# Kernel tuning notes

Hardware: AMD Instinct MI355X
Metric: run time of the kernel (lower is better)

The kernel has to match this reference:

```python
import jax, jax.numpy as jnp
import numpy as np

N, M, F, B = 100000, 12, 64, 41  # atoms, max neighbors, atom feat dim, bond feat dim
EPS = 1e-5


def setup_inputs() -> dict:
    key = jax.random.key(0)
    ks = jax.random.split(key, 8)
    neighbor_indices = jax.random.randint(ks[0], (N, M), 0, N, dtype=jnp.int32)
    atom_features = jax.random.normal(ks[1], (N, F), dtype=jnp.float32)
    bond_features = jax.random.normal(ks[2], (N, M, B), dtype=jnp.float32)
    W = jax.random.normal(ks[3], (2 * F + B, 2 * F), dtype=jnp.float32) * 0.05
    b = jnp.zeros((2 * F,), dtype=jnp.float32)
    bn1_scale = 1.0 + 0.02 * jax.random.normal(ks[4], (2 * F,), dtype=jnp.float32)
    bn1_offset = 0.02 * jax.random.normal(ks[5], (2 * F,), dtype=jnp.float32)
    bn2_scale = 1.0 + 0.02 * jax.random.normal(ks[6], (F,), dtype=jnp.float32)
    bn2_offset = 0.02 * jax.random.normal(ks[7], (F,), dtype=jnp.float32)
    return {"neighbor_indices": neighbor_indices, "atom_features": atom_features,
            "bond_features": bond_features, "W": W, "b": b,
            "bn1_scale": bn1_scale, "bn1_offset": bn1_offset,
            "bn2_scale": bn2_scale, "bn2_offset": bn2_offset}


def batchnorm(x, scale, offset):
    # haiku BatchNorm, training mode: batch stats over all axes but channel (last)
    mean = jnp.mean(x, axis=0, keepdims=True)
    var = jnp.mean(jnp.square(x), axis=0, keepdims=True) - jnp.square(mean)
    inv = scale * jax.lax.rsqrt(var + EPS)
    return (x - mean) * inv + offset


def reference(neighbor_indices, atom_features, bond_features, W, b,
              bn1_scale, bn1_offset, bn2_scale, bn2_offset):
    n = atom_features.shape[0]
    nbr_feats = atom_features[neighbor_indices]  # (N, M, F) gather
    self_feats = jnp.broadcast_to(atom_features[:, None, :], (n, M, F))
    total = jnp.concatenate([self_feats, nbr_feats, bond_features], axis=2)  # (N, M, 2F+B)
    gated = total @ W + b  # (N, M, 2F)
    gated = batchnorm(gated.reshape(-1, 2 * F), bn1_scale, bn1_offset).reshape(n, M, 2 * F)
    nbr_filter, nbr_core = jnp.split(gated, 2, axis=2)
    summed = jnp.sum(jax.nn.sigmoid(nbr_filter) * jax.nn.softplus(nbr_core), axis=1)  # (N, F)
    summed = batchnorm(summed, bn2_scale, bn2_offset)
    return jax.nn.softplus(atom_features + summed)
```

## Files before the change

### kernel.cpp

```cpp
#include <hip/hip_runtime.h>
#include <hip/hip_bf16.h>
#include <math.h>


#define NATOMS  100000
#define MNBR    12
#define FDIM    64
#define BDIM    41
#define C2F     128
#define EPSBN   1e-5f
#define NBLK    2048
#define GROUPS  (NATOMS/4)
#define AR      136
#define PR      72

typedef __attribute__((ext_vector_type(8))) short  short8;
typedef __attribute__((ext_vector_type(4))) float  f32x4;

__device__ __forceinline__ float softplusf(float x) {
    return fmaxf(x, 0.f) + __logf(1.f + __expf(-fabsf(x)));
}
__device__ __forceinline__ float sigmoidf(float x) {
    return 1.f / (1.f + __expf(-x));
}
__device__ __forceinline__ unsigned short f2bf(float f) {
    unsigned int x = __builtin_bit_cast(unsigned int, f);
    unsigned int r = (x + 0x7fff + ((x >> 16) & 1)) >> 16;
    return (unsigned short)r;
}
__device__ __forceinline__ unsigned int pkbf(float a, float b) {
    unsigned short lo = __builtin_bit_cast(unsigned short, __float2bfloat16(a));
    unsigned short hi = __builtin_bit_cast(unsigned short, __float2bfloat16(b));
    return (unsigned)lo | ((unsigned)hi << 16);
}
__device__ __forceinline__ float bflo(unsigned int u) {
    return __builtin_bit_cast(float, u << 16);
}
__device__ __forceinline__ float bfhi(unsigned int u) {
    return __builtin_bit_cast(float, u & 0xffff0000u);
}
__device__ __forceinline__ float bf2f(unsigned short u) {
    return __builtin_bit_cast(float, ((unsigned int)u) << 16);
}

__global__ __launch_bounds__(256) void k_pack(
    const float* __restrict__ W,
    unsigned short* __restrict__ Wsn, unsigned short* __restrict__ Wpk)
{
    const int t0 = blockIdx.x*256 + threadIdx.x;
    for (int idx = t0; idx < 8*2*64*8; idx += gridDim.x*256) {
        int e = idx & 7, lane = (idx >> 3) & 63, ks = (idx >> 9) & 1, n = idx >> 10;
        int k   = ks*32 + (lane >> 4)*8 + e;
        int col = n*16 + (lane & 15);
        Wsn[idx] = f2bf(W[k*C2F + col]);
    }
    for (int idx = t0; idx < 8*4*64*8; idx += gridDim.x*256) {
        int e = idx & 7, lane = (idx >> 3) & 63, ks = (idx >> 9) & 3, n = idx >> 11;
        int k   = ks*32 + (lane >> 4)*8 + e;
        int col = n*16 + (lane & 15);
        float v = (k < 105) ? W[(64 + k)*C2F + col] : 0.f;
        Wpk[idx] = f2bf(v);
    }
}

__global__ __launch_bounds__(256, 4) void k_proj(
    const float* __restrict__ atomF, const unsigned short* __restrict__ Wsn,
    unsigned short* __restrict__ PselfBf, unsigned short* __restrict__ atomBf)
{
    __shared__ __align__(16) unsigned short A[64*PR];
    const int tid = threadIdx.x, w = tid >> 6, lane = tid & 63;
    const int g = lane >> 4, x = lane & 15;
    short8 B0[2], B1[2];
    #pragma unroll
    for (int ks = 0; ks < 2; ++ks) {
        B0[ks] = *(const short8*)(Wsn + ((w*2 + ks)*64 + lane)*8);
        B1[ks] = *(const short8*)(Wsn + (((w+4)*2 + ks)*64 + lane)*8);
    }
    for (int a0 = blockIdx.x*64; a0 < NATOMS; a0 += gridDim.x*64) {
        __syncthreads();
        #pragma unroll
        for (int it = 0; it < 4; ++it) {
            int idx = it*256 + tid;
            int p = idx >> 4, c = idx & 15;
            int i = a0 + p;
            float4 v = make_float4(0.f, 0.f, 0.f, 0.f);
            if (i < NATOMS) v = *(const float4*)(atomF + (size_t)i*FDIM + 4*c);
            uint2 u; u.x = pkbf(v.x, v.y); u.y = pkbf(v.z, v.w);
            *(uint2*)(A + p*PR + 4*c) = u;
            if (i < NATOMS) *(uint2*)(atomBf + (size_t)i*FDIM + 4*c) = u;
        }
        __syncthreads();
        f32x4 z = {0.f, 0.f, 0.f, 0.f};
        f32x4 acc[4][2];
        #pragma unroll
        for (int m = 0; m < 4; ++m) { acc[m][0] = z; acc[m][1] = z; }
        #pragma unroll
        for (int ks = 0; ks < 2; ++ks) {
            #pragma unroll
            for (int m = 0; m < 4; ++m) {
                short8 a = *(const short8*)(A + (m*16 + x)*PR + ks*32 + g*8);
                acc[m][0] = __builtin_amdgcn_mfma_f32_16x16x32_bf16(a, B0[ks], acc[m][0], 0, 0, 0);
                acc[m][1] = __builtin_amdgcn_mfma_f32_16x16x32_bf16(a, B1[ks], acc[m][1], 0, 0, 0);
            }
        }
        #pragma unroll
        for (int m = 0; m < 4; ++m) {
            int i = a0 + m*16 + g*4;
            #pragma unroll
            for (int rg = 0; rg < 4; ++rg) {
                if (i + rg < NATOMS) {
                    PselfBf[(size_t)(i+rg)*C2F + w*16 + x]     = f2bf(acc[m][0][rg]);
                    PselfBf[(size_t)(i+rg)*C2F + (w+4)*16 + x] = f2bf(acc[m][1][rg]);
                }
            }
        }
    }
}

__global__ __launch_bounds__(256, 4) void k_gemm(
    const int* __restrict__ nbr, const unsigned short* __restrict__ atomBf,
    const float* __restrict__ bond, const unsigned short* __restrict__ Wpk,
    const unsigned short* __restrict__ PselfBf,
    uint4* __restrict__ gated, float* __restrict__ partial1)
{
    __shared__ __align__(16) unsigned short A[2][48*AR];
    const int tid = threadIdx.x, w = tid >> 6, lane = tid & 63;
    const int g = lane >> 4, x = lane & 15;
    const int ch0 = w*16 + x;
    short8 B0[4], B1[4];
    #pragma unroll
    for (int ks = 0; ks < 4; ++ks) {
        B0[ks] = *(const short8*)(Wpk + ((w*4 + ks)*64 + lane)*8);
        B1[ks] = *(const short8*)(Wpk + (((w+4)*4 + ks)*64 + lane)*8);
    }
    for (int idx = tid; idx < 2*48*AR/2; idx += 256) ((unsigned int*)A)[idx] = 0u;

    uint2 st[6];
    float s0 = 0.f, q0 = 0.f, s1 = 0.f, q1 = 0.f;

#define LOADG(GRP)                                                            \
    {   const int base_ = (GRP)*4;                                            \
        _Pragma("unroll")                                                     \
        for (int it = 0; it < 6; ++it) {                                      \
            int idx = it*256 + tid;                                           \
            int p = idx >> 5, c = idx & 31;                                   \
            if (c < 16) {                                                     \
                int r = nbr[base_*MNBR + p];                                  \
                st[it] = *(const uint2*)(atomBf + ((size_t)r << 6) + 4*c);    \
            } else if (c < 27) {                                              \
                int cc = c - 16;                                              \
                int pa = p/12;                                                \
                const float* bp = bond + (size_t)(base_ + pa)*(MNBR*BDIM)     \
                                       + (p - pa*12)*BDIM + 4*cc;             \
                float b0 = bp[0], b1 = 0.f, b2 = 0.f, b3 = 0.f;               \
                if (cc < 10) { b1 = bp[1]; b2 = bp[2]; b3 = bp[3]; }          \
                st[it].x = pkbf(b0, b1); st[it].y = pkbf(b2, b3);             \
            }                                                                 \
        } }

#define WRITEA(BUF)                                                           \
    {   _Pragma("unroll")                                                     \
        for (int it = 0; it < 6; ++it) {                                      \
            int idx = it*256 + tid;                                           \
            int p = idx >> 5, c = idx & 31;                                   \
            if (c < 16)      *(uint2*)(&A[BUF][p*AR + 4*c]) = st[it];         \
            else if (c < 27) *(uint2*)(&A[BUF][p*AR + 64 + 4*(c-16)]) = st[it]; \
        } }

    int grp = blockIdx.x;
    int cur = 0;
    if (grp < GROUPS) { LOADG(grp); WRITEA(0); }
    for (; grp < GROUPS; grp += gridDim.x) {
        const int nxt = grp + gridDim.x;
        __syncthreads();
        if (nxt < GROUPS) LOADG(nxt);
        f32x4 z = {0.f, 0.f, 0.f, 0.f};
        f32x4 acc[3][2];
        #pragma unroll
        for (int m = 0; m < 3; ++m) { acc[m][0] = z; acc[m][1] = z; }
        #pragma unroll
        for (int ks = 0; ks < 4; ++ks) {
            #pragma unroll
            for (int m = 0; m < 3; ++m) {
                short8 a = *(const short8*)(&A[cur][(m*16 + x)*AR + ks*32 + g*8]);
                acc[m][0] = __builtin_amdgcn_mfma_f32_16x16x32_bf16(a, B0[ks], acc[m][0], 0, 0, 0);
                acc[m][1] = __builtin_amdgcn_mfma_f32_16x16x32_bf16(a, B1[ks], acc[m][1], 0, 0, 0);
            }
        }
        const int base = grp*4;
        uint4* gbase = gated + ((size_t)grp*4 + w)*3*64 + lane;
        #pragma unroll
        for (int m = 0; m < 3; ++m) {
            int ia = base + (m*16 + g*4)/12;
            float ps0 = bf2f(PselfBf[(size_t)ia*C2F + ch0]);
            float ps1 = bf2f(PselfBf[(size_t)ia*C2F + 64 + ch0]);
            float v00 = acc[m][0][0] + ps0, v01 = acc[m][0][1] + ps0;
            float v02 = acc[m][0][2] + ps0, v03 = acc[m][0][3] + ps0;
            float v10 = acc[m][1][0] + ps1, v11 = acc[m][1][1] + ps1;
            float v12 = acc[m][1][2] + ps1, v13 = acc[m][1][3] + ps1;
            s0 += (v00 + v01) + (v02 + v03);
            s1 += (v10 + v11) + (v12 + v13);
            q0 = fmaf(v00, v00, q0); q0 = fmaf(v01, v01, q0);
            q0 = fmaf(v02, v02, q0); q0 = fmaf(v03, v03, q0);
            q1 = fmaf(v10, v10, q1); q1 = fmaf(v11, v11, q1);
            q1 = fmaf(v12, v12, q1); q1 = fmaf(v13, v13, q1);
            uint4 pk;
            pk.x = pkbf(v00, v01); pk.y = pkbf(v02, v03);
            pk.z = pkbf(v10, v11); pk.w = pkbf(v12, v13);
            gbase[m*64] = pk;
        }
        if (nxt < GROUPS) WRITEA(cur ^ 1);
        cur ^= 1;
    }
#undef LOADG
#undef WRITEA
    s0 += __shfl_xor(s0, 16); s0 += __shfl_xor(s0, 32);
    s1 += __shfl_xor(s1, 16); s1 += __shfl_xor(s1, 32);
    q0 += __shfl_xor(q0, 16); q0 += __shfl_xor(q0, 32);
    q1 += __shfl_xor(q1, 16); q1 += __shfl_xor(q1, 32);
    if (g == 0) {
        float* pb = partial1 + blockIdx.x*256;
        pb[ch0]            = s0; pb[64 + ch0]        = s1;
        pb[C2F + ch0]      = q0; pb[C2F + 64 + ch0]  = q1;
    }
}

__global__ __launch_bounds__(256) void k_red(
    const float* __restrict__ in, float* __restrict__ outp, int width)
{
    const int b = blockIdx.x;
    for (int c = threadIdx.x; c < width; c += 256) {
        float s = 0.f;
        #pragma unroll 4
        for (int k = 0; k < 16; ++k) s += in[(size_t)(b*16 + k)*width + c];
        outp[(size_t)b*width + c] = s;
    }
}

__global__ __launch_bounds__(1024) void k_bn1_finalize(
    const float* __restrict__ red1, const float* __restrict__ scale,
    const float* __restrict__ offset, float* __restrict__ prm1)
{
    __shared__ float redS[1024], redQ[1024];
    const int tid = threadIdx.x, c = tid & 127, h = tid >> 7;
    float S = 0.f, Q = 0.f;
    for (int blk = h; blk < 128; blk += 8) {
        S += red1[blk*256 + c];
        Q += red1[blk*256 + 128 + c];
    }
    redS[tid] = S; redQ[tid] = Q;
    __syncthreads();
    if (tid < 128) {
        float Sa = 0.f, Qa = 0.f;
        #pragma unroll
        for (int hh = 0; hh < 8; ++hh) { Sa += redS[hh*128 + c]; Qa += redQ[hh*128 + c]; }
        const float invn = 1.f / (float)(NATOMS * MNBR);
        float mean = Sa * invn;
        float var  = Qa * invn - mean*mean;
        float inv  = scale[c] * rsqrtf(var + EPSBN);
        prm1[c]       = inv;
        prm1[128 + c] = offset[c] - mean*inv;
    }
}

__global__ __launch_bounds__(256, 8) void k_apply(
    const uint4* __restrict__ gated, const float* __restrict__ prm1,
    float* __restrict__ summed, float* __restrict__ partial2)
{
    __shared__ float Y[12*66];
    __shared__ float red[256];
    const int tid = threadIdx.x, w = tid >> 6, lane = tid & 63;
    const int g = lane >> 4, x = lane & 15;
    const int ch0 = w*16 + x;
    const float iv0 = prm1[ch0],      of0 = prm1[C2F + ch0];
    const float iv1 = prm1[64 + ch0], of1 = prm1[C2F + 64 + ch0];
    float s2 = 0.f, q2 = 0.f;

    for (int grp = blockIdx.x; grp < GROUPS; grp += gridDim.x) {
        __syncthreads();
        const uint4* gbase = gated + ((size_t)grp*4 + w)*3*64 + lane;
        #pragma unroll
        for (int m = 0; m < 3; ++m) {
            uint4 pk = gbase[m*64];
            float y00 = bflo(pk.x)*iv0 + of0, y01 = bfhi(pk.x)*iv0 + of0;
            float y02 = bflo(pk.y)*iv0 + of0, y03 = bfhi(pk.y)*iv0 + of0;
            float y10 = bflo(pk.z)*iv1 + of1, y11 = bfhi(pk.z)*iv1 + of1;
            float y12 = bflo(pk.w)*iv1 + of1, y13 = bfhi(pk.w)*iv1 + of1;
            float sY = sigmoidf(y00)*softplusf(y10) + sigmoidf(y01)*softplusf(y11)
                     + sigmoidf(y02)*softplusf(y12) + sigmoidf(y03)*softplusf(y13);
            Y[(m*4 + g)*66 + ch0] = sY;
        }
        __syncthreads();
        float sv = Y[(3*w)*66 + lane] + Y[(3*w + 1)*66 + lane] + Y[(3*w + 2)*66 + lane];
        summed[(size_t)(grp*4 + w)*FDIM + lane] = sv;
        s2 += sv; q2 = fmaf(sv, sv, q2);
    }
    red[tid] = s2; __syncthreads();
    if (tid < 64) partial2[blockIdx.x*128 + tid]
        = red[tid] + red[tid+64] + red[tid+128] + red[tid+192];
    __syncthreads();
    red[tid] = q2; __syncthreads();
    if (tid < 64) partial2[blockIdx.x*128 + 64 + tid]
        = red[tid] + red[tid+64] + red[tid+128] + red[tid+192];
}

__global__ __launch_bounds__(1024) void k_bn2_finalize(
    const float* __restrict__ red2, const float* __restrict__ scale,
    const float* __restrict__ offset, float* __restrict__ prm2)
{
    __shared__ float redS[1024], redQ[1024];
    const int tid = threadIdx.x, f = tid & 63, h = tid >> 6;
    float S = 0.f, Q = 0.f;
    for (int blk = h; blk < 128; blk += 16) {
        S += red2[blk*128 + f];
        Q += red2[blk*128 + 64 + f];
    }
    redS[tid] = S; redQ[tid] = Q;
    __syncthreads();
    if (tid < 64) {
        float Sa = 0.f, Qa = 0.f;
        #pragma unroll
        for (int hh = 0; hh < 16; ++hh) { Sa += redS[hh*64 + f]; Qa += redQ[hh*64 + f]; }
        const float invn = 1.f / (float)NATOMS;
        float mean = Sa * invn;
        float var  = Qa * invn - mean*mean;
        float inv  = scale[f] * rsqrtf(var + EPSBN);
        prm2[f]      = inv;
        prm2[64 + f] = offset[f] - mean*inv;
    }
}

__global__ __launch_bounds__(256) void k_final(
    const float* __restrict__ atomF, const float* __restrict__ summed,
    const float* __restrict__ prm2, float* __restrict__ out)
{
    __shared__ float iv[64], of[64];
    if (threadIdx.x < 64) {
        iv[threadIdx.x] = prm2[threadIdx.x];
        of[threadIdx.x] = prm2[64 + threadIdx.x];
    }
    __syncthreads();
    const int total4 = NATOMS*FDIM/4;
    for (int t = blockIdx.x*blockDim.x + threadIdx.x; t < total4;
         t += gridDim.x*blockDim.x) {
        float4 a = ((const float4*)atomF)[t];
        float4 s = ((const float4*)summed)[t];
        int fb = (t*4) & 63;
        float4 r;
        r.x = softplusf(a.x + s.x*iv[fb]   + of[fb]);
        r.y = softplusf(a.y + s.y*iv[fb+1] + of[fb+1]);
        r.z = softplusf(a.z + s.z*iv[fb+2] + of[fb+2]);
        r.w = softplusf(a.w + s.w*iv[fb+3] + of[fb+3]);
        ((float4*)out)[t] = r;
    }
}

extern "C" void kernel_launch(void* const* d_in, const int* in_sizes, int n_in,
                              void* d_out, int out_size, void* d_ws, size_t ws_size,
                              hipStream_t stream)
{
    const int*   nbr   = (const int*)  d_in[0];
    const float* atomF = (const float*)d_in[1];
    const float* bond  = (const float*)d_in[2];
    const float* W     = (const float*)d_in[3];
    const float* s1    = (const float*)d_in[5];
    const float* o1    = (const float*)d_in[6];
    const float* s2    = (const float*)d_in[7];
    const float* o2    = (const float*)d_in[8];
    float* out = (float*)d_out;

    uint4* gated        = (uint4*)d_ws;
    unsigned short* PselfBf = (unsigned short*)(gated + (size_t)GROUPS*12*64);
    unsigned short* atomBf  = PselfBf + (size_t)NATOMS*C2F;
    float* summed   = (float*)(atomBf + (size_t)NATOMS*FDIM);
    float* partial1 = summed   + (size_t)NATOMS*FDIM;
    float* partial2 = partial1 + (size_t)NBLK*256;
    float* red1     = partial2 + (size_t)NBLK*128;
    float* red2     = red1     + 128*256;
    float* prm1     = red2     + 128*128;
    float* prm2     = prm1     + 256;
    unsigned short* Wsn = (unsigned short*)(prm2 + 128);
    unsigned short* Wpk = Wsn + 8192;

    hipLaunchKernelGGL(k_pack,         dim3(64),   dim3(256),  0, stream, W, Wsn, Wpk);
    hipLaunchKernelGGL(k_proj,         dim3(782),  dim3(256),  0, stream,
                       atomF, Wsn, PselfBf, atomBf);
    hipLaunchKernelGGL(k_gemm,         dim3(NBLK), dim3(256),  0, stream,
                       nbr, atomBf, bond, Wpk, PselfBf, gated, partial1);
    hipLaunchKernelGGL(k_red,          dim3(128),  dim3(256),  0, stream, partial1, red1, 256);
    hipLaunchKernelGGL(k_bn1_finalize, dim3(1),    dim3(1024), 0, stream, red1, s1, o1, prm1);
    hipLaunchKernelGGL(k_apply,        dim3(NBLK), dim3(256),  0, stream,
                       gated, prm1, summed, partial2);
    hipLaunchKernelGGL(k_red,          dim3(128),  dim3(256),  0, stream, partial2, red2, 128);
    hipLaunchKernelGGL(k_bn2_finalize, dim3(1),    dim3(1024), 0, stream, red2, s2, o2, prm2);
    hipLaunchKernelGGL(k_final,        dim3(2048), dim3(256),  0, stream, atomF, summed, prm2, out);
}
```

Measured before the change: 394.2 us.

## Precompute per-atom neighbor projection and recompute gated values instead of storing them

The neighbor-feature part of the matmul is split out algebraically: each atom's projection through the neighbor rows of W is computed once per atom in k_proj, and each edge then gathers a 128-wide bf16 row instead of doing that GEMM slice itself. The per-edge MFMA then covers only the bond features (K=41, padded to 64). The gated intermediate tensor is no longer written. Instead, both the stats pass and the apply pass recompute the bond GEMM and gather projections, which removes a large write and read of gated data in exchange for reading bond features twice and doing two scattered gathers per edge. NBLK, the LDS row stride and the occupancy bounds are adjusted to match.

```diff
diff --git a/kernel.cpp b/kernel.cpp
--- a/kernel.cpp
+++ b/kernel.cpp
@@ -9,9 +9,9 @@
 #define BDIM    41
 #define C2F     128
 #define EPSBN   1e-5f
-#define NBLK    2048
+#define NBLK    1280
 #define GROUPS  (NATOMS/4)
-#define AR      136
+#define AR      72
 #define PR      72
 
 typedef __attribute__((ext_vector_type(8))) short  short8;
@@ -33,48 +33,45 @@
     unsigned short hi = __builtin_bit_cast(unsigned short, __float2bfloat16(b));
     return (unsigned)lo | ((unsigned)hi << 16);
 }
-__device__ __forceinline__ float bflo(unsigned int u) {
-    return __builtin_bit_cast(float, u << 16);
-}
-__device__ __forceinline__ float bfhi(unsigned int u) {
-    return __builtin_bit_cast(float, u & 0xffff0000u);
-}
 __device__ __forceinline__ float bf2f(unsigned short u) {
     return __builtin_bit_cast(float, ((unsigned int)u) << 16);
 }
 
 __global__ __launch_bounds__(256) void k_pack(
     const float* __restrict__ W,
-    unsigned short* __restrict__ Wsn, unsigned short* __restrict__ Wpk)
+    unsigned short* __restrict__ Wal, unsigned short* __restrict__ Wbd)
 {
     const int t0 = blockIdx.x*256 + threadIdx.x;
+    for (int idx = t0; idx < 2*8*2*64*8; idx += gridDim.x*256) {
+        int e = idx & 7, lane = (idx >> 3) & 63, ks = (idx >> 9) & 1;
+        int n = (idx >> 10) & 7, h = idx >> 13;
+        int k   = h*64 + ks*32 + (lane >> 4)*8 + e;
+        int col = n*16 + (lane & 15);
+        Wal[idx] = f2bf(W[k*C2F + col]);
+    }
     for (int idx = t0; idx < 8*2*64*8; idx += gridDim.x*256) {
         int e = idx & 7, lane = (idx >> 3) & 63, ks = (idx >> 9) & 1, n = idx >> 10;
-        int k   = ks*32 + (lane >> 4)*8 + e;
+        int kk  = ks*32 + (lane >> 4)*8 + e;
         int col = n*16 + (lane & 15);
-        Wsn[idx] = f2bf(W[k*C2F + col]);
-    }
-    for (int idx = t0; idx < 8*4*64*8; idx += gridDim.x*256) {
-        int e = idx & 7, lane = (idx >> 3) & 63, ks = (idx >> 9) & 3, n = idx >> 11;
-        int k   = ks*32 + (lane >> 4)*8 + e;
-        int col = n*16 + (lane & 15);
-        float v = (k < 105) ? W[(64 + k)*C2F + col] : 0.f;
-        Wpk[idx] = f2bf(v);
+        float v = (kk < BDIM) ? W[(2*FDIM + kk)*C2F + col] : 0.f;
+        Wbd[idx] = f2bf(v);
     }
 }
 
 __global__ __launch_bounds__(256, 4) void k_proj(
-    const float* __restrict__ atomF, const unsigned short* __restrict__ Wsn,
-    unsigned short* __restrict__ PselfBf, unsigned short* __restrict__ atomBf)
+    const float* __restrict__ atomF, const unsigned short* __restrict__ Wal,
+    unsigned short* __restrict__ PselfBf, unsigned short* __restrict__ PnbrBf)
 {
     __shared__ __align__(16) unsigned short A[64*PR];
     const int tid = threadIdx.x, w = tid >> 6, lane = tid & 63;
     const int g = lane >> 4, x = lane & 15;
-    short8 B0[2], B1[2];
+    short8 Bs0[2], Bs1[2], Bn0[2], Bn1[2];
     #pragma unroll
     for (int ks = 0; ks < 2; ++ks) {
-        B0[ks] = *(const short8*)(Wsn + ((w*2 + ks)*64 + lane)*8);
-        B1[ks] = *(const short8*)(Wsn + (((w+4)*2 + ks)*64 + lane)*8);
+        Bs0[ks] = *(const short8*)(Wal + (((0*8 + w    )*2 + ks)*64 + lane)*8);
+        Bs1[ks] = *(const short8*)(Wal + (((0*8 + w + 4)*2 + ks)*64 + lane)*8);
+        Bn0[ks] = *(const short8*)(Wal + (((1*8 + w    )*2 + ks)*64 + lane)*8);
+        Bn1[ks] = *(const short8*)(Wal + (((1*8 + w + 4)*2 + ks)*64 + lane)*8);
     }
     for (int a0 = blockIdx.x*64; a0 < NATOMS; a0 += gridDim.x*64) {
         __syncthreads();
@@ -87,20 +84,22 @@
             if (i < NATOMS) v = *(const float4*)(atomF + (size_t)i*FDIM + 4*c);
             uint2 u; u.x = pkbf(v.x, v.y); u.y = pkbf(v.z, v.w);
             *(uint2*)(A + p*PR + 4*c) = u;
-            if (i < NATOMS) *(uint2*)(atomBf + (size_t)i*FDIM + 4*c) = u;
         }
         __syncthreads();
         f32x4 z = {0.f, 0.f, 0.f, 0.f};
-        f32x4 acc[4][2];
-        #pragma unroll
-        for (int m = 0; m < 4; ++m) { acc[m][0] = z; acc[m][1] = z; }
+        f32x4 acc[4][4];
+        #pragma unroll
+        for (int m = 0; m < 4; ++m)
+            { acc[m][0] = z; acc[m][1] = z; acc[m][2] = z; acc[m][3] = z; }
         #pragma unroll
         for (int ks = 0; ks < 2; ++ks) {
             #pragma unroll
             for (int m = 0; m < 4; ++m) {
                 short8 a = *(const short8*)(A + (m*16 + x)*PR + ks*32 + g*8);
-                acc[m][0] = __builtin_amdgcn_mfma_f32_16x16x32_bf16(a, B0[ks], acc[m][0], 0, 0, 0);
-                acc[m][1] = __builtin_amdgcn_mfma_f32_16x16x32_bf16(a, B1[ks], acc[m][1], 0, 0, 0);
+                acc[m][0] = __builtin_amdgcn_mfma_f32_16x16x32_bf16(a, Bs0[ks], acc[m][0], 0, 0, 0);
+                acc[m][1] = __builtin_amdgcn_mfma_f32_16x16x32_bf16(a, Bs1[ks], acc[m][1], 0, 0, 0);
+                acc[m][2] = __builtin_amdgcn_mfma_f32_16x16x32_bf16(a, Bn0[ks], acc[m][2], 0, 0, 0);
+                acc[m][3] = __builtin_amdgcn_mfma_f32_16x16x32_bf16(a, Bn1[ks], acc[m][3], 0, 0, 0);
             }
         }
         #pragma unroll
@@ -109,62 +108,59 @@
             #pragma unroll
             for (int rg = 0; rg < 4; ++rg) {
                 if (i + rg < NATOMS) {
-                    PselfBf[(size_t)(i+rg)*C2F + w*16 + x]     = f2bf(acc[m][0][rg]);
-                    PselfBf[(size_t)(i+rg)*C2F + (w+4)*16 + x] = f2bf(acc[m][1][rg]);
+                    size_t o = (size_t)(i+rg)*C2F;
+                    PselfBf[o + w*16 + x]       = f2bf(acc[m][0][rg]);
+                    PselfBf[o + (w+4)*16 + x]   = f2bf(acc[m][1][rg]);
+                    PnbrBf [o + w*16 + x]       = f2bf(acc[m][2][rg]);
+                    PnbrBf [o + (w+4)*16 + x]   = f2bf(acc[m][3][rg]);
                 }
             }
         }
     }
 }
 
-__global__ __launch_bounds__(256, 4) void k_gemm(
-    const int* __restrict__ nbr, const unsigned short* __restrict__ atomBf,
-    const float* __restrict__ bond, const unsigned short* __restrict__ Wpk,
+
+__global__ __launch_bounds__(256, 5) void k_stats(
+    const int* __restrict__ nbr, const float* __restrict__ bond,
+    const unsigned short* __restrict__ Wbd,
     const unsigned short* __restrict__ PselfBf,
-    uint4* __restrict__ gated, float* __restrict__ partial1)
+    const unsigned short* __restrict__ PnbrBf,
+    float* __restrict__ partial1)
 {
     __shared__ __align__(16) unsigned short A[2][48*AR];
     const int tid = threadIdx.x, w = tid >> 6, lane = tid & 63;
     const int g = lane >> 4, x = lane & 15;
     const int ch0 = w*16 + x;
-    short8 B0[4], B1[4];
+    short8 B0[2], B1[2];
     #pragma unroll
-    for (int ks = 0; ks < 4; ++ks) {
-        B0[ks] = *(const short8*)(Wpk + ((w*4 + ks)*64 + lane)*8);
-        B1[ks] = *(const short8*)(Wpk + (((w+4)*4 + ks)*64 + lane)*8);
+    for (int ks = 0; ks < 2; ++ks) {
+        B0[ks] = *(const short8*)(Wbd + ((w*2 + ks)*64 + lane)*8);
+        B1[ks] = *(const short8*)(Wbd + (((w+4)*2 + ks)*64 + lane)*8);
     }
     for (int idx = tid; idx < 2*48*AR/2; idx += 256) ((unsigned int*)A)[idx] = 0u;
-
-    uint2 st[6];
+    uint2 st[3];
     float s0 = 0.f, q0 = 0.f, s1 = 0.f, q1 = 0.f;
 
 #define LOADG(GRP)                                                            \
     {   const int base_ = (GRP)*4;                                            \
         _Pragma("unroll")                                                     \
-        for (int it = 0; it < 6; ++it) {                                      \
+        for (int it = 0; it < 3; ++it) {                                      \
             int idx = it*256 + tid;                                           \
-            int p = idx >> 5, c = idx & 31;                                   \
-            if (c < 16) {                                                     \
-                int r = nbr[base_*MNBR + p];                                  \
-                st[it] = *(const uint2*)(atomBf + ((size_t)r << 6) + 4*c);    \
-            } else if (c < 27) {                                              \
-                int cc = c - 16;                                              \
-                int pa = p/12;                                                \
-                const float* bp = bond + (size_t)(base_ + pa)*(MNBR*BDIM)     \
-                                       + (p - pa*12)*BDIM + 4*cc;             \
+            int p = idx >> 4, c = idx & 15;                                   \
+            if (c < 11) {                                                     \
+                const float* bp = bond + (size_t)base_*(MNBR*BDIM)            \
+                                       + p*BDIM + 4*c;                        \
                 float b0 = bp[0], b1 = 0.f, b2 = 0.f, b3 = 0.f;               \
-                if (cc < 10) { b1 = bp[1]; b2 = bp[2]; b3 = bp[3]; }          \
+                if (c < 10) { b1 = bp[1]; b2 = bp[2]; b3 = bp[3]; }           \
                 st[it].x = pkbf(b0, b1); st[it].y = pkbf(b2, b3);             \
             }                                                                 \
         } }
-
 #define WRITEA(BUF)                                                           \
     {   _Pragma("unroll")                                                     \
-        for (int it = 0; it < 6; ++it) {                                      \
+        for (int it = 0; it < 3; ++it) {                                      \
             int idx = it*256 + tid;                                           \
-            int p = idx >> 5, c = idx & 31;                                   \
-            if (c < 16)      *(uint2*)(&A[BUF][p*AR + 4*c]) = st[it];         \
-            else if (c < 27) *(uint2*)(&A[BUF][p*AR + 64 + 4*(c-16)]) = st[it]; \
+            int p = idx >> 4, c = idx & 15;                                   \
+            if (c < 11) *(uint2*)(&A[BUF][p*AR + 4*c]) = st[it];              \
         } }
 
     int grp = blockIdx.x;
@@ -172,14 +168,24 @@
     if (grp < GROUPS) { LOADG(grp); WRITEA(0); }
     for (; grp < GROUPS; grp += gridDim.x) {
         const int nxt = grp + gridDim.x;
+        const int base = grp*4;
         __syncthreads();
+        int4 ridx[3];
+        float ps0[3], ps1[3];
+        #pragma unroll
+        for (int m = 0; m < 3; ++m) {
+            ridx[m] = *(const int4*)(nbr + base*MNBR + m*16 + g*4);
+            int ia = base + (m*16 + g*4)/12;
+            ps0[m] = bf2f(PselfBf[(size_t)ia*C2F + ch0]);
+            ps1[m] = bf2f(PselfBf[(size_t)ia*C2F + 64 + ch0]);
+        }
         if (nxt < GROUPS) LOADG(nxt);
         f32x4 z = {0.f, 0.f, 0.f, 0.f};
         f32x4 acc[3][2];
         #pragma unroll
         for (int m = 0; m < 3; ++m) { acc[m][0] = z; acc[m][1] = z; }
         #pragma unroll
-        for (int ks = 0; ks < 4; ++ks) {
+        for (int ks = 0; ks < 2; ++ks) {
             #pragma unroll
             for (int m = 0; m < 3; ++m) {
                 short8 a = *(const short8*)(&A[cur][(m*16 + x)*AR + ks*32 + g*8]);
@@ -187,33 +193,21 @@
                 acc[m][1] = __builtin_amdgcn_mfma_f32_16x16x32_bf16(a, B1[ks], acc[m][1], 0, 0, 0);
             }
         }
-        const int base = grp*4;
-        uint4* gbase = gated + ((size_t)grp*4 + w)*3*64 + lane;
         #pragma unroll
         for (int m = 0; m < 3; ++m) {
-            int ia = base + (m*16 + g*4)/12;
-            float ps0 = bf2f(PselfBf[(size_t)ia*C2F + ch0]);
-            float ps1 = bf2f(PselfBf[(size_t)ia*C2F + 64 + ch0]);
-            float v00 = acc[m][0][0] + ps0, v01 = acc[m][0][1] + ps0;
-            float v02 = acc[m][0][2] + ps0, v03 = acc[m][0][3] + ps0;
-            float v10 = acc[m][1][0] + ps1, v11 = acc[m][1][1] + ps1;
-            float v12 = acc[m][1][2] + ps1, v13 = acc[m][1][3] + ps1;
-            s0 += (v00 + v01) + (v02 + v03);
-            s1 += (v10 + v11) + (v12 + v13);
-            q0 = fmaf(v00, v00, q0); q0 = fmaf(v01, v01, q0);
-            q0 = fmaf(v02, v02, q0); q0 = fmaf(v03, v03, q0);
-            q1 = fmaf(v10, v10, q1); q1 = fmaf(v11, v11, q1);
-            q1 = fmaf(v12, v12, q1); q1 = fmaf(v13, v13, q1);
-            uint4 pk;
-            pk.x = pkbf(v00, v01); pk.y = pkbf(v02, v03);
-            pk.z = pkbf(v10, v11); pk.w = pkbf(v12, v13);
-            gbase[m*64] = pk;
+            const int rr[4] = {ridx[m].x, ridx[m].y, ridx[m].z, ridx[m].w};
+            #pragma unroll
+            for (int rg = 0; rg < 4; ++rg) {
+                size_t o = (size_t)rr[rg]*C2F;
+                float v0 = acc[m][0][rg] + ps0[m] + bf2f(PnbrBf[o + ch0]);
+                float v1 = acc[m][1][rg] + ps1[m] + bf2f(PnbrBf[o + 64 + ch0]);
+                s0 += v0; q0 = fmaf(v0, v0, q0);
+                s1 += v1; q1 = fmaf(v1, v1, q1);
+            }
         }
         if (nxt < GROUPS) WRITEA(cur ^ 1);
         cur ^= 1;
     }
-#undef LOADG
-#undef WRITEA
     s0 += __shfl_xor(s0, 16); s0 += __shfl_xor(s0, 32);
     s1 += __shfl_xor(s1, 16); s1 += __shfl_xor(s1, 32);
     q0 += __shfl_xor(q0, 16); q0 += __shfl_xor(q0, 32);
@@ -231,8 +225,8 @@
     const int b = blockIdx.x;
     for (int c = threadIdx.x; c < width; c += 256) {
         float s = 0.f;
-        #pragma unroll 4
-        for (int k = 0; k < 16; ++k) s += in[(size_t)(b*16 + k)*width + c];
+        #pragma unroll
+        for (int k = 0; k < NBLK/128; ++k) s += in[(size_t)(b*(NBLK/128) + k)*width + c];
         outp[(size_t)b*width + c] = s;
     }
 }
@@ -263,38 +257,86 @@
     }
 }
 
-__global__ __launch_bounds__(256, 8) void k_apply(
-    const uint4* __restrict__ gated, const float* __restrict__ prm1,
+__global__ __launch_bounds__(256, 5) void k_apply(
+    const int* __restrict__ nbr, const float* __restrict__ bond,
+    const unsigned short* __restrict__ Wbd,
+    const unsigned short* __restrict__ PselfBf,
+    const unsigned short* __restrict__ PnbrBf,
+    const float* __restrict__ prm1,
     float* __restrict__ summed, float* __restrict__ partial2)
 {
+    __shared__ __align__(16) unsigned short A[2][48*AR];
     __shared__ float Y[12*66];
     __shared__ float red[256];
     const int tid = threadIdx.x, w = tid >> 6, lane = tid & 63;
     const int g = lane >> 4, x = lane & 15;
     const int ch0 = w*16 + x;
+    short8 B0[2], B1[2];
+    #pragma unroll
+    for (int ks = 0; ks < 2; ++ks) {
+        B0[ks] = *(const short8*)(Wbd + ((w*2 + ks)*64 + lane)*8);
+        B1[ks] = *(const short8*)(Wbd + (((w+4)*2 + ks)*64 + lane)*8);
+    }
     const float iv0 = prm1[ch0],      of0 = prm1[C2F + ch0];
     const float iv1 = prm1[64 + ch0], of1 = prm1[C2F + 64 + ch0];
+    for (int idx = tid; idx < 2*48*AR/2; idx += 256) ((unsigned int*)A)[idx] = 0u;
+    uint2 st[3];
     float s2 = 0.f, q2 = 0.f;
 
-    for (int grp = blockIdx.x; grp < GROUPS; grp += gridDim.x) {
+    int grp = blockIdx.x;
+    int cur = 0;
+    if (grp < GROUPS) { LOADG(grp); WRITEA(0); }
+    for (; grp < GROUPS; grp += gridDim.x) {
+        const int nxt = grp + gridDim.x;
+        const int base = grp*4;
         __syncthreads();
-        const uint4* gbase = gated + ((size_t)grp*4 + w)*3*64 + lane;
+        int4 ridx[3];
+        float ps0[3], ps1[3];
         #pragma unroll
         for (int m = 0; m < 3; ++m) {
-            uint4 pk = gbase[m*64];
-            float y00 = bflo(pk.x)*iv0 + of0, y01 = bfhi(pk.x)*iv0 + of0;
-            float y02 = bflo(pk.y)*iv0 + of0, y03 = bfhi(pk.y)*iv0 + of0;
-            float y10 = bflo(pk.z)*iv1 + of1, y11 = bfhi(pk.z)*iv1 + of1;
-            float y12 = bflo(pk.w)*iv1 + of1, y13 = bfhi(pk.w)*iv1 + of1;
-            float sY = sigmoidf(y00)*softplusf(y10) + sigmoidf(y01)*softplusf(y11)
-                     + sigmoidf(y02)*softplusf(y12) + sigmoidf(y03)*softplusf(y13);
+            ridx[m] = *(const int4*)(nbr + base*MNBR + m*16 + g*4);
+            int ia = base + (m*16 + g*4)/12;
+            ps0[m] = bf2f(PselfBf[(size_t)ia*C2F + ch0]);
+            ps1[m] = bf2f(PselfBf[(size_t)ia*C2F + 64 + ch0]);
+        }
+        if (nxt < GROUPS) LOADG(nxt);
+        f32x4 z = {0.f, 0.f, 0.f, 0.f};
+        f32x4 acc[3][2];
+        #pragma unroll
+        for (int m = 0; m < 3; ++m) { acc[m][0] = z; acc[m][1] = z; }
+        #pragma unroll
+        for (int ks = 0; ks < 2; ++ks) {
+            #pragma unroll
+            for (int m = 0; m < 3; ++m) {
+                short8 a = *(const short8*)(&A[cur][(m*16 + x)*AR + ks*32 + g*8]);
+                acc[m][0] = __builtin_amdgcn_mfma_f32_16x16x32_bf16(a, B0[ks], acc[m][0], 0, 0, 0);
+                acc[m][1] = __builtin_amdgcn_mfma_f32_16x16x32_bf16(a, B1[ks], acc[m][1], 0, 0, 0);
+            }
+        }
+        #pragma unroll
+        for (int m = 0; m < 3; ++m) {
+            const int rr[4] = {ridx[m].x, ridx[m].y, ridx[m].z, ridx[m].w};
+            float sY = 0.f;
+            #pragma unroll
+            for (int rg = 0; rg < 4; ++rg) {
+                size_t o = (size_t)rr[rg]*C2F;
+                float v0 = acc[m][0][rg] + ps0[m] + bf2f(PnbrBf[o + ch0]);
+                float v1 = acc[m][1][rg] + ps1[m] + bf2f(PnbrBf[o + 64 + ch0]);
+                float y0 = v0*iv0 + of0;
+                float y1 = v1*iv1 + of1;
+                sY += sigmoidf(y0) * softplusf(y1);
+            }
             Y[(m*4 + g)*66 + ch0] = sY;
         }
         __syncthreads();
         float sv = Y[(3*w)*66 + lane] + Y[(3*w + 1)*66 + lane] + Y[(3*w + 2)*66 + lane];
-        summed[(size_t)(grp*4 + w)*FDIM + lane] = sv;
+        summed[(size_t)(base + w)*FDIM + lane] = sv;
         s2 += sv; q2 = fmaf(sv, sv, q2);
-    }
+        if (nxt < GROUPS) WRITEA(cur ^ 1);
+        cur ^= 1;
+    }
+#undef LOADG
+#undef WRITEA
     red[tid] = s2; __syncthreads();
     if (tid < 64) partial2[blockIdx.x*128 + tid]
         = red[tid] + red[tid+64] + red[tid+128] + red[tid+192];
@@ -369,28 +411,27 @@
     const float* o2    = (const float*)d_in[8];
     float* out = (float*)d_out;
 
-    uint4* gated        = (uint4*)d_ws;
-    unsigned short* PselfBf = (unsigned short*)(gated + (size_t)GROUPS*12*64);
-    unsigned short* atomBf  = PselfBf + (size_t)NATOMS*C2F;
-    float* summed   = (float*)(atomBf + (size_t)NATOMS*FDIM);
+    unsigned short* PselfBf = (unsigned short*)d_ws;
+    unsigned short* PnbrBf  = PselfBf + (size_t)NATOMS*C2F;
+    float* summed   = (float*)(PnbrBf + (size_t)NATOMS*C2F);
     float* partial1 = summed   + (size_t)NATOMS*FDIM;
     float* partial2 = partial1 + (size_t)NBLK*256;
     float* red1     = partial2 + (size_t)NBLK*128;
     float* red2     = red1     + 128*256;
     float* prm1     = red2     + 128*128;
     float* prm2     = prm1     + 256;
-    unsigned short* Wsn = (unsigned short*)(prm2 + 128);
-    unsigned short* Wpk = Wsn + 8192;
-
-    hipLaunchKernelGGL(k_pack,         dim3(64),   dim3(256),  0, stream, W, Wsn, Wpk);
-    hipLaunchKernelGGL(k_proj,         dim3(782),  dim3(256),  0, stream,
-                       atomF, Wsn, PselfBf, atomBf);
-    hipLaunchKernelGGL(k_gemm,         dim3(NBLK), dim3(256),  0, stream,
-                       nbr, atomBf, bond, Wpk, PselfBf, gated, partial1);
+    unsigned short* Wal = (unsigned short*)(prm2 + 128);
+    unsigned short* Wbd = Wal + 16384;
+
+    hipLaunchKernelGGL(k_pack,         dim3(64),   dim3(256),  0, stream, W, Wal, Wbd);
+    hipLaunchKernelGGL(k_proj,         dim3(1024), dim3(256),  0, stream,
+                       atomF, Wal, PselfBf, PnbrBf);
+    hipLaunchKernelGGL(k_stats,        dim3(NBLK), dim3(256),  0, stream,
+                       nbr, bond, Wbd, PselfBf, PnbrBf, partial1);
     hipLaunchKernelGGL(k_red,          dim3(128),  dim3(256),  0, stream, partial1, red1, 256);
     hipLaunchKernelGGL(k_bn1_finalize, dim3(1),    dim3(1024), 0, stream, red1, s1, o1, prm1);
     hipLaunchKernelGGL(k_apply,        dim3(NBLK), dim3(256),  0, stream,
-                       gated, prm1, summed, partial2);
+                       nbr, bond, Wbd, PselfBf, PnbrBf, prm1, summed, partial2);
     hipLaunchKernelGGL(k_red,          dim3(128),  dim3(256),  0, stream, partial2, red2, 128);
     hipLaunchKernelGGL(k_bn2_finalize, dim3(1),    dim3(1024), 0, stream, red2, s2, o2, prm2);
     hipLaunchKernelGGL(k_final,        dim3(2048), dim3(256),  0, stream, atomF, summed, prm2, out);
```

After: 448.0 us. 13.6% more time.
